# Kernel tuning notes

Measured on AMD Instinct MI355X. Metric: run time of the kernel, lower is better.

## Reference

```python
import jax, jax.numpy as jnp
import numpy as np

REL_LEN = 100  # self.relative_length in the module
LN_EPS = 1e-3  # tf.keras LayerNormalization default epsilon


def sinusoid_table(rel_len, d):
    # position_encoding_relative: sinusoid over relative offsets -L..L, [2L+1, d]
    pos = jnp.arange(-rel_len, rel_len + 1, dtype=jnp.float32)[:, None]
    i = jnp.arange(d // 2, dtype=jnp.float32)[None, :]
    inv_freq = jnp.exp(-jnp.log(10000.0) * (2.0 * i) / d)
    ang = pos * inv_freq
    return jnp.concatenate([jnp.sin(ang), jnp.cos(ang)], axis=-1)


def setup_inputs() -> dict:
    key = jax.random.key(0)
    B, S, E, HID, H = 4, 512, 512, 2048, 8
    ks = jax.random.split(key, 16)
    g = lambda k, sh: jax.random.normal(k, sh, jnp.float32) / jnp.sqrt(jnp.float32(sh[0]))
    return {
        "values": jax.random.normal(ks[0], (B, S, E), jnp.float32),
        "values_mask": jnp.ones((B, S), dtype=bool),
        "rel_enc": sinusoid_table(REL_LEN, E),            # [201, E]
        "ln0_g": jnp.ones((E,), jnp.float32), "ln0_b": jnp.zeros((E,), jnp.float32),
        "w_b0": g(ks[1], (E, HID)), "b_b0": jnp.zeros((HID,), jnp.float32),
        "wq": g(ks[2], (HID, E)), "bq": jnp.zeros((E,), jnp.float32),
        "wke": g(ks[3], (HID, E)), "bke": jnp.zeros((E,), jnp.float32),
        "wkv": g(ks[4], (HID, E)), "bkv": jnp.zeros((E,), jnp.float32),
        "wkr": g(ks[5], (E, E)), "bkr": jnp.zeros((E,), jnp.float32),
        "wab0": g(ks[6], (E, H)), "bab0": jnp.zeros((H,), jnp.float32),
        "wab1": g(ks[7], (E, H)), "bab1": jnp.zeros((H,), jnp.float32),
        "ln1_g": jnp.ones((E,), jnp.float32), "ln1_b": jnp.zeros((E,), jnp.float32),
        "w11": g(ks[8], (E, HID)), "b11": jnp.zeros((HID,), jnp.float32),
        "w12": g(ks[9], (HID, E)), "b12": jnp.zeros((E,), jnp.float32),
    }


def _ln(x, g, b):
    m = jnp.mean(x, -1, keepdims=True)
    v = jnp.var(x, -1, keepdims=True)
    return (x - m) * jax.lax.rsqrt(v + LN_EPS) * g + b


def reference(values, values_mask, rel_enc, ln0_g, ln0_b, w_b0, b_b0,
              wq, bq, wke, bke, wkv, bkv, wkr, bkr,
              wab0, bab0, wab1, bab1, ln1_g, ln1_b, w11, b11, w12, b12):
    B, S, E = values.shape
    H = wab0.shape[1]
    D = E // H
    # block0 (lastfc=False): LayerNorm -> Dense(hidden, relu)
    x = jax.nn.relu(_ln(values, ln0_g, ln0_b) @ w_b0 + b_b0)          # [B,S,HID]
    q = x @ wq + bq                                                    # [B,S,E]
    ke = x @ wke + bke
    kv = x @ wkv + bkv
    # relative encodings: gather = one-hot rel map @ encoding table
    offs = jnp.clip(jnp.arange(S)[None, :] - jnp.arange(S)[:, None], -REL_LEN, REL_LEN) + REL_LEN
    rel = rel_enc[offs]                                                # [S,S,E]
    kr = rel @ wkr + bkr                                               # [S,S,E]
    # learned bias terms
    bias0 = (ke @ wab0 + bab0).transpose(0, 2, 1)[:, :, None, :]       # [B,H,1,S]
    bias1 = (kr @ wab1 + bab1).transpose(2, 0, 1)[None]                # [1,H,S,S]
    tr = lambda u: u.reshape(B, S, H, D).transpose(0, 2, 1, 3)         # [B,H,S,D]
    qh, keh, kvh = tr(q), tr(ke), tr(kv)
    krh = kr.reshape(S, S, H, D).transpose(2, 0, 1, 3)                 # [H,S,S,D]
    # q . kr content-position term, contracted without [B,H,S,S,D] materialization
    biasprod = jnp.einsum('bhid,hijd->bhij', qh, krh)                  # [B,H,S,S]
    bias = biasprod + bias0 + bias1
    # AttentionWithBias: scaled dot product + bias, key mask + causal mask
    logits = jnp.einsum('bhid,bhjd->bhij', qh, keh) / jnp.sqrt(jnp.float32(D)) + bias
    causal = jnp.tril(jnp.ones((S, S), dtype=bool))[None, None]        # [1,1,S,S]
    keymask = values_mask[:, None, None, :]                            # [B,1,1,S]
    logits = jnp.where(causal & keymask, logits, jnp.float32(-1e9))
    scores = jax.nn.softmax(logits, axis=-1)
    att = jnp.einsum('bhij,bhjd->bhid', scores, kvh)                   # [B,H,S,D]
    att = att.transpose(0, 2, 1, 3).reshape(B, S, E)
    v = values + att
    # block1: LayerNorm -> Dense(hidden, relu) -> Dense(input_size)
    y = jax.nn.relu(_ln(v, ln1_g, ln1_b) @ w11 + b11) @ w12 + b12
    return v + y
```

## Files before the change

kernel.cpp:

```cpp
#include <hip/hip_runtime.h>
#include <hip/hip_bf16.h>
#include <cstddef>
#include <cstdint>

#define LN_EPS 0.001f

using short8 = __attribute__((ext_vector_type(8))) short;
using f32x4 = __attribute__((ext_vector_type(4))) float;

#define GLOAD_LDS16(gp, lp)                                                    \
  __builtin_amdgcn_global_load_lds(                                            \
      (const __attribute__((address_space(1))) void*)(gp),                     \
      (__attribute__((address_space(3))) void*)(lp), 16, 0, 0)

static __device__ __forceinline__ short f2bf(float x) {
  __hip_bfloat16 h = __float2bfloat16(x);
  return *reinterpret_cast<short*>(&h);
}

__global__ __launch_bounds__(256) void prep_ln_kernel(
    const float* __restrict__ w_b0, const float* __restrict__ w11,
    const float* __restrict__ wq, const float* __restrict__ wke,
    const float* __restrict__ wkv, const float* __restrict__ w12,
    const float* __restrict__ wkr, const float* __restrict__ rel_enc,
    __hip_bfloat16* __restrict__ w_b0t, __hip_bfloat16* __restrict__ w11t,
    __hip_bfloat16* __restrict__ wqt, __hip_bfloat16* __restrict__ wket,
    __hip_bfloat16* __restrict__ wkvt, __hip_bfloat16* __restrict__ w12t,
    __hip_bfloat16* __restrict__ wkrt, __hip_bfloat16* __restrict__ relb,
    const float* __restrict__ lnx, const float* __restrict__ lng,
    const float* __restrict__ lnb, __hip_bfloat16* __restrict__ lnout) {
  int bid = blockIdx.x;
  int t = threadIdx.x;
  if (bid >= 6656) {
    int row = bid - 6656;
    const float* xr = lnx + (size_t)row * 512;
    float v0 = xr[t], v1 = xr[t + 256];
    float s = v0 + v1, sq = v0 * v0 + v1 * v1;
#pragma unroll
    for (int o = 32; o; o >>= 1) {
      s += __shfl_down(s, o);
      sq += __shfl_down(sq, o);
    }
    __shared__ float wsum[4], wsq[4];
    __shared__ float mean_s, scale_s;
    int wid = t >> 6, lane = t & 63;
    if (lane == 0) { wsum[wid] = s; wsq[wid] = sq; }
    __syncthreads();
    if (t == 0) {
      float S = wsum[0] + wsum[1] + wsum[2] + wsum[3];
      float SQ = wsq[0] + wsq[1] + wsq[2] + wsq[3];
      float mean = S * (1.f / 512.f);
      float var = SQ * (1.f / 512.f) - mean * mean;
      mean_s = mean;
      scale_s = rsqrtf(var + LN_EPS);
    }
    __syncthreads();
    float mean = mean_s, scale = scale_s;
    __hip_bfloat16* orow = lnout + (size_t)row * 512;
    orow[t] = __float2bfloat16((v0 - mean) * scale * lng[t] + lnb[t]);
    orow[t + 256] = __float2bfloat16((v1 - mean) * scale * lng[t + 256] + lnb[t + 256]);
    return;
  }
  if (bid >= 6400) {
    int row = bid - 6400;
    float v0 = 0.f, v1 = 0.f;
    if (row < 201) {
      v0 = rel_enc[(size_t)row * 512 + t];
      v1 = rel_enc[(size_t)row * 512 + t + 256];
    }
    relb[(size_t)row * 512 + t] = __float2bfloat16(v0);
    relb[(size_t)row * 512 + t + 256] = __float2bfloat16(v1);
    return;
  }
  const float* in;
  __hip_bfloat16* outp;
  int R, C, bx, by;
  if (bid < 6144) {
    int seg = bid >> 10, idx = bid & 1023;
    if (seg == 0)      { in = w_b0; outp = w_b0t; R = 512;  C = 2048; }
    else if (seg == 1) { in = w11;  outp = w11t;  R = 512;  C = 2048; }
    else if (seg == 2) { in = wq;   outp = wqt;   R = 2048; C = 512;  }
    else if (seg == 3) { in = wke;  outp = wket;  R = 2048; C = 512;  }
    else if (seg == 4) { in = wkv;  outp = wkvt;  R = 2048; C = 512;  }
    else               { in = w12;  outp = w12t;  R = 2048; C = 512;  }
    if (R == 512) { bx = idx & 63; by = idx >> 6; }
    else          { bx = idx & 15; by = idx >> 4; }
  } else {
    int idx = bid - 6144;
    in = wkr; outp = wkrt; R = 512; C = 512;
    bx = idx & 15; by = idx >> 4;
  }
  __shared__ float tile[32][33];
  int c0 = bx * 32, r0 = by * 32;
  int tx = t & 31, ty = t >> 5;
#pragma unroll
  for (int p = 0; p < 4; p++) {
    int r = ty + p * 8;
    tile[r][tx] = in[(size_t)(r0 + r) * C + c0 + tx];
  }
  __syncthreads();
#pragma unroll
  for (int p = 0; p < 4; p++) {
    int r = ty + p * 8;
    outp[(size_t)(c0 + r) * R + r0 + tx] = __float2bfloat16(tile[tx][r]);
  }
}

__global__ __launch_bounds__(256) void ln_kernel(const float* __restrict__ x,
                                                 const float* __restrict__ g,
                                                 const float* __restrict__ bb,
                                                 __hip_bfloat16* __restrict__ out) {
  int row = blockIdx.x;
  const float* xr = x + (size_t)row * 512;
  int t = threadIdx.x;
  float v0 = xr[t], v1 = xr[t + 256];
  float s = v0 + v1, sq = v0 * v0 + v1 * v1;
#pragma unroll
  for (int o = 32; o; o >>= 1) {
    s += __shfl_down(s, o);
    sq += __shfl_down(sq, o);
  }
  __shared__ float wsum[4], wsq[4];
  __shared__ float mean_s, scale_s;
  int wid = t >> 6, lane = t & 63;
  if (lane == 0) { wsum[wid] = s; wsq[wid] = sq; }
  __syncthreads();
  if (t == 0) {
    float S = wsum[0] + wsum[1] + wsum[2] + wsum[3];
    float SQ = wsq[0] + wsq[1] + wsq[2] + wsq[3];
    float mean = S * (1.f / 512.f);
    float var = SQ * (1.f / 512.f) - mean * mean;
    mean_s = mean;
    scale_s = rsqrtf(var + LN_EPS);
  }
  __syncthreads();
  float mean = mean_s, scale = scale_s;
  __hip_bfloat16* orow = out + (size_t)row * 512;
  orow[t] = __float2bfloat16((v0 - mean) * scale * g[t] + bb[t]);
  orow[t + 256] = __float2bfloat16((v1 - mean) * scale * g[t + 256] + bb[t + 256]);
}

template <int TM, int TN, int MODE, int RELU, int RESID>
__global__ __launch_bounds__(256) void gemm_mfma(
    const __hip_bfloat16* __restrict__ A, const __hip_bfloat16* __restrict__ Bt,
    const float* __restrict__ bias0, const float* __restrict__ bias1,
    const float* __restrict__ bias2, const float* __restrict__ resid,
    void* __restrict__ out0, void* __restrict__ out1, void* __restrict__ out2,
    int M, int N, int K,
    const __hip_bfloat16* A2, const __hip_bfloat16* B2t,
    const float* bias_kr, void* out_kr, int ysplit) {
  constexpr int FM = TM / 32;
  constexpr int FN = TN / 32;
  __shared__ short As[2][TM * 64];
  __shared__ short Bs[2][TN * 64];
  int tid = threadIdx.x;
  int w = tid >> 6, lane = tid & 63;
  int wrow = (w >> 1) * (TM / 2);
  int wcol = (w & 1) * (TN / 2);
  int quad = lane >> 4, l16 = lane & 15;
  int bx = blockIdx.x, by = blockIdx.y;
  const short* Ag = (const short*)A;
  const short* Bg = (const short*)Bt;
  int N_ = N, K_ = K;
  bool is_kr = false;
  if (MODE == 1 && ysplit > 0 && by >= ysplit) {
    if (bx >= 512 / TN) return;
    is_kr = true;
    by -= ysplit;
    Ag = (const short*)A2;
    Bg = (const short*)B2t;
    N_ = 512;
    K_ = 512;
  }
  int row0 = by * TM, col0 = bx * TN;
  f32x4 acc[FM][FN];
#pragma unroll
  for (int i = 0; i < FM; i++)
#pragma unroll
    for (int j = 0; j < FN; j++) acc[i][j] = {0.f, 0.f, 0.f, 0.f};

  auto stage = [&](int k0, int buf) {
#pragma unroll
    for (int p = 0; p < TM / 32; p++) {
      int e = p * 256 + tid;
      int r = e >> 3, sc = e & 7;
      int c = sc ^ (r & 7);
      GLOAD_LDS16(Ag + (size_t)(row0 + r) * K_ + k0 + c * 8, &As[buf][e * 8]);
    }
#pragma unroll
    for (int p = 0; p < TN / 32; p++) {
      int e = p * 256 + tid;
      int r = e >> 3, sc = e & 7;
      int c = sc ^ (r & 7);
      GLOAD_LDS16(Bg + (size_t)(col0 + r) * K_ + k0 + c * 8, &Bs[buf][e * 8]);
    }
  };

  int nIter = K_ >> 6;
  stage(0, 0);
  for (int it = 0; it < nIter; ++it) {
    int cur = it & 1;
    __syncthreads();
    if (it + 1 < nIter) stage((it + 1) << 6, cur ^ 1);
#pragma unroll
    for (int u = 0; u < 2; u++) {
      short8 af[FM], bf[FN];
#pragma unroll
      for (int f = 0; f < FM; f++) {
        int r = wrow + f * 16 + l16;
        int slot = (u * 4 + quad) ^ (r & 7);
        af[f] = *(const short8*)&As[cur][(r * 8 + slot) * 8];
      }
#pragma unroll
      for (int f = 0; f < FN; f++) {
        int r = wcol + f * 16 + l16;
        int slot = (u * 4 + quad) ^ (r & 7);
        bf[f] = *(const short8*)&Bs[cur][(r * 8 + slot) * 8];
      }
#pragma unroll
      for (int fm = 0; fm < FM; fm++)
#pragma unroll
        for (int fn = 0; fn < FN; fn++)
          acc[fm][fn] = __builtin_amdgcn_mfma_f32_16x16x32_bf16(af[fm], bf[fn], acc[fm][fn], 0, 0, 0);
    }
  }

  int seg = 0;
  const float* bp = is_kr ? bias_kr : bias0;
  __hip_bfloat16* opb = nullptr;
  if (MODE == 2) {
    seg = col0 >> 9;
    bp = (seg == 0) ? bias0 : (seg == 1 ? bias1 : bias2);
    opb = (__hip_bfloat16*)((seg == 0) ? out0 : out1);
  }
#pragma unroll
  for (int fm = 0; fm < FM; fm++) {
#pragma unroll
    for (int fn = 0; fn < FN; fn++) {
      int gc = col0 + wcol + fn * 16 + l16;
      int bcol = (MODE == 2) ? (gc - seg * 512) : gc;
      float bv = bp[bcol];
#pragma unroll
      for (int r = 0; r < 4; r++) {
        int gr = row0 + wrow + fm * 16 + quad * 4 + r;
        float v = acc[fm][fn][r] + bv;
        if (RELU && !is_kr) v = fmaxf(v, 0.f);
        if (MODE == 0) {
          size_t idx = (size_t)gr * N_ + gc;
          if (RESID) v += resid[idx];
          ((float*)out0)[idx] = v;
        } else if (MODE == 1) {
          __hip_bfloat16* dst = is_kr ? (__hip_bfloat16*)out_kr : (__hip_bfloat16*)out0;
          dst[(size_t)gr * N_ + gc] = __float2bfloat16(v);
        } else {
          if (seg < 2) {
            opb[(size_t)gr * 512 + bcol] = __float2bfloat16(v);
          } else {
            int b_ = gr >> 9, s_ = gr & 511;
            int h_ = bcol >> 6, d_ = bcol & 63;
            ((__hip_bfloat16*)out2)[(size_t)((b_ * 8 + h_) * 64 + d_) * 512 + s_] =
                __float2bfloat16(v);
          }
        }
      }
    }
  }
}

__global__ void rowdot_merged(const __hip_bfloat16* __restrict__ ke,
                              const __hip_bfloat16* __restrict__ krtb,
                              const float* __restrict__ wab0, const float* __restrict__ bab0,
                              const float* __restrict__ wab1, const float* __restrict__ bab1,
                              float* __restrict__ keab, float* __restrict__ b1t) {
  int bid = blockIdx.x;
  int lane = threadIdx.x;
  int second = (bid >= 2048);
  int r = second ? (bid - 2048) : bid;
  const __hip_bfloat16* ar = (second ? krtb : ke) + (size_t)r * 512;
  const float* W = second ? wab1 : wab0;
  const float* bb = second ? bab1 : bab0;
  float a[8];
#pragma unroll
  for (int u = 0; u < 8; u++) a[u] = __bfloat162float(ar[lane + u * 64]);
  float s[8] = {0.f, 0.f, 0.f, 0.f, 0.f, 0.f, 0.f, 0.f};
#pragma unroll
  for (int u = 0; u < 8; u++) {
    int e = lane + u * 64;
    const float4* w4 = (const float4*)&W[(size_t)e * 8];
    float4 w0 = w4[0], w1 = w4[1];
    s[0] += a[u] * w0.x; s[1] += a[u] * w0.y; s[2] += a[u] * w0.z; s[3] += a[u] * w0.w;
    s[4] += a[u] * w1.x; s[5] += a[u] * w1.y; s[6] += a[u] * w1.z; s[7] += a[u] * w1.w;
  }
#pragma unroll
  for (int h = 0; h < 8; h++) {
    float v = s[h];
#pragma unroll
    for (int o = 1; o < 64; o <<= 1) v += __shfl_xor(v, o);
    if (lane == h) {
      if (!second) {
        int b_ = r >> 9, s_ = r & 511;
        keab[(size_t)(b_ * 8 + h) * 512 + s_] = v + bb[h];
      } else {
        b1t[(size_t)r * 8 + h] = v + bb[h];
      }
    }
  }
}

#define PST 136
__global__ __launch_bounds__(256) void attn_mfma4(
    const __hip_bfloat16* __restrict__ q, const __hip_bfloat16* __restrict__ ke,
    const __hip_bfloat16* __restrict__ kvt, const __hip_bfloat16* __restrict__ krtb,
    const float* __restrict__ keab, const float* __restrict__ b1t,
    const float* __restrict__ values, float* __restrict__ v_out) {
  const int S = 512, E = 512;
  __shared__ float bp[16 * 113];
  __shared__ short P[4][16 * PST];
  __shared__ float ml[4][32];
  int tid = threadIdx.x;
  int wave = tid >> 6, lane = tid & 63;
  int quad = lane >> 4, l16 = lane & 15;
  int band = 31 - blockIdx.x;
  int h = blockIdx.y, b = blockIdx.z;
  int wi0 = band * 16;

  const short* qg = (const short*)q;
  const short* keg = (const short*)ke;
  const short* kvtg = (const short*)kvt;
  const short* krg = (const short*)krtb;

  short8 aq[2];
#pragma unroll
  for (int kk = 0; kk < 2; kk++)
    aq[kk] = *(const short8*)&qg[(size_t)(b * S + wi0 + l16) * E + h * 64 + kk * 32 + quad * 8];

#pragma unroll
  for (int oi = 0; oi < 2; oi++) {
    int on = wave + oi * 4;
    if (on < 7) {
      f32x4 c = {0.f, 0.f, 0.f, 0.f};
#pragma unroll
      for (int kk = 0; kk < 2; kk++) {
        short8 bfr = *(const short8*)&krg[(size_t)(on * 16 + l16) * E + h * 64 + kk * 32 + quad * 8];
        c = __builtin_amdgcn_mfma_f32_16x16x32_bf16(aq[kk], bfr, c, 0, 0, 0);
      }
      float b1 = b1t[(on * 16 + l16) * 8 + h];
#pragma unroll
      for (int rr = 0; rr < 4; rr++)
        bp[(quad * 4 + rr) * 113 + on * 16 + l16] = c[rr] + b1;
    }
  }
  __syncthreads();

  int nb = (band >= wave) ? (((band - wave) >> 2) + 1) : 0;

  f32x4 s[8];
  const float* keabh = keab + (size_t)(b * 8 + h) * 512;
#pragma unroll
  for (int t = 0; t < 8; t++) {
    if (t < nb) {
      int j = (4 * t + wave) * 16 + l16;
      f32x4 c = {0.f, 0.f, 0.f, 0.f};
#pragma unroll
      for (int kk = 0; kk < 2; kk++) {
        short8 bk = *(const short8*)&keg[(size_t)(b * S + j) * E + h * 64 + kk * 32 + quad * 8];
        c = __builtin_amdgcn_mfma_f32_16x16x32_bf16(aq[kk], bk, c, 0, 0, 0);
      }
      float ka = keabh[j];
#pragma unroll
      for (int rr = 0; rr < 4; rr++) {
        int i = wi0 + quad * 4 + rr;
        float val = -1e30f;
        if (j <= i) {
          int off = j - i + 100;
          if (off < 0) off = 0;
          val = c[rr] * 0.125f + bp[(quad * 4 + rr) * 113 + off] + ka;
        }
        s[t][rr] = val;
      }
    }
  }

  float m_r[4] = {-1e30f, -1e30f, -1e30f, -1e30f};
#pragma unroll
  for (int t = 0; t < 8; t++)
    if (t < nb)
#pragma unroll
      for (int rr = 0; rr < 4; rr++) m_r[rr] = fmaxf(m_r[rr], s[t][rr]);
#pragma unroll
  for (int rr = 0; rr < 4; rr++) {
    float v = m_r[rr];
    v = fmaxf(v, __shfl_xor(v, 1));
    v = fmaxf(v, __shfl_xor(v, 2));
    v = fmaxf(v, __shfl_xor(v, 4));
    v = fmaxf(v, __shfl_xor(v, 8));
    m_r[rr] = v;
  }
  float l_r[4] = {0.f, 0.f, 0.f, 0.f};
  short* Pw = &P[wave][0];
#pragma unroll
  for (int t = 0; t < 8; t++) {
    if (t < nb) {
#pragma unroll
      for (int rr = 0; rr < 4; rr++) {
        float p = __expf(s[t][rr] - m_r[rr]);
        l_r[rr] += p;
        Pw[(quad * 4 + rr) * PST + t * 16 + l16] = f2bf(p);
      }
    }
  }
  if (nb & 1) {
#pragma unroll
    for (int rr = 0; rr < 4; rr++)
      Pw[(quad * 4 + rr) * PST + nb * 16 + l16] = 0;
  }
#pragma unroll
  for (int rr = 0; rr < 4; rr++) {
    float v = l_r[rr];
    v += __shfl_xor(v, 1);
    v += __shfl_xor(v, 2);
    v += __shfl_xor(v, 4);
    v += __shfl_xor(v, 8);
    l_r[rr] = v;
  }

  f32x4 o[4] = {{0.f,0.f,0.f,0.f},{0.f,0.f,0.f,0.f},{0.f,0.f,0.f,0.f},{0.f,0.f,0.f,0.f}};
  int nkk = (nb + 1) >> 1;
  const short* kvbase = &kvtg[(size_t)(b * 8 + h) * 64 * S];
#pragma unroll
  for (int kk = 0; kk < 4; kk++) {
    if (kk < nkk) {
      short8 ap = *(const short8*)&Pw[l16 * PST + kk * 32 + quad * 8];
      int jgl = (4 * (2 * kk + (quad >> 1)) + wave) * 16 + (quad & 1) * 8;
#pragma unroll
      for (int dn = 0; dn < 4; dn++) {
        short8 bv = *(const short8*)&kvbase[(size_t)(dn * 16 + l16) * S + jgl];
        o[dn] = __builtin_amdgcn_mfma_f32_16x16x32_bf16(ap, bv, o[dn], 0, 0, 0);
      }
    }
  }

  float* omw = (float*)&P[wave][0];
#pragma unroll
  for (int rr = 0; rr < 4; rr++) {
    int row = quad * 4 + rr;
    if (l16 == 0) {
      ml[wave][row * 2] = m_r[rr];
      ml[wave][row * 2 + 1] = l_r[rr];
    }
#pragma unroll
    for (int dn = 0; dn < 4; dn++)
      omw[row * 68 + dn * 16 + l16] = o[dn][rr];
  }
  __syncthreads();
  int dn = wave;
#pragma unroll
  for (int rr = 0; rr < 4; rr++) {
    int row = quad * 4 + rr;
    float ms = -1e30f;
#pragma unroll
    for (int wv = 0; wv < 4; wv++) ms = fmaxf(ms, ml[wv][row * 2]);
    float lsum = 0.f, oo = 0.f;
    int col = dn * 16 + l16;
#pragma unroll
    for (int wv = 0; wv < 4; wv++) {
      float aw = __expf(ml[wv][row * 2] - ms);
      lsum += ml[wv][row * 2 + 1] * aw;
      oo += ((float*)&P[wv][0])[row * 68 + col] * aw;
    }
    oo /= lsum;
    size_t idx = (size_t)(b * S + wi0 + row) * E + h * 64 + col;
    v_out[idx] = values[idx] + oo;
  }
}

extern "C" void kernel_launch(void* const* d_in, const int* in_sizes, int n_in,
                              void* d_out, int out_size, void* d_ws, size_t ws_size,
                              hipStream_t stream) {
  const float* values = (const float*)d_in[0];
  const float* rel_enc = (const float*)d_in[2];
  const float* ln0_g = (const float*)d_in[3];
  const float* ln0_b = (const float*)d_in[4];
  const float* w_b0 = (const float*)d_in[5];
  const float* b_b0 = (const float*)d_in[6];
  const float* wq = (const float*)d_in[7];
  const float* bq = (const float*)d_in[8];
  const float* wke = (const float*)d_in[9];
  const float* bke = (const float*)d_in[10];
  const float* wkv = (const float*)d_in[11];
  const float* bkv = (const float*)d_in[12];
  const float* wkr = (const float*)d_in[13];
  const float* bkr = (const float*)d_in[14];
  const float* wab0 = (const float*)d_in[15];
  const float* bab0 = (const float*)d_in[16];
  const float* wab1 = (const float*)d_in[17];
  const float* bab1 = (const float*)d_in[18];
  const float* ln1_g = (const float*)d_in[19];
  const float* ln1_b = (const float*)d_in[20];
  const float* w11 = (const float*)d_in[21];
  const float* b11 = (const float*)d_in[22];
  const float* w12 = (const float*)d_in[23];
  const float* b12 = (const float*)d_in[24];
  float* out = (float*)d_out;

  char* p = (char*)d_ws;
  __hip_bfloat16* buf_ln = (__hip_bfloat16*)p;  p += (size_t)2048 * 512 * 2;
  __hip_bfloat16* x      = (__hip_bfloat16*)p;  p += (size_t)2048 * 2048 * 2;
  __hip_bfloat16* q      = (__hip_bfloat16*)p;  p += (size_t)2048 * 512 * 2;
  __hip_bfloat16* ke     = (__hip_bfloat16*)p;  p += (size_t)2048 * 512 * 2;
  __hip_bfloat16* kvt    = (__hip_bfloat16*)p;  p += (size_t)2048 * 512 * 2;
  float* v    = (float*)p;                      p += (size_t)2048 * 512 * 4;
  __hip_bfloat16* krtb = (__hip_bfloat16*)p;    p += (size_t)256 * 512 * 2;
  __hip_bfloat16* relb = (__hip_bfloat16*)p;    p += (size_t)256 * 512 * 2;
  __hip_bfloat16* wkrt = (__hip_bfloat16*)p;    p += (size_t)512 * 512 * 2;
  float* keab = (float*)p;                      p += (size_t)4 * 8 * 512 * 4;
  float* b1t  = (float*)p;                      p += (size_t)208 * 8 * 4;
  __hip_bfloat16* w_b0t = (__hip_bfloat16*)p;   p += (size_t)2048 * 512 * 2;
  __hip_bfloat16* wcatt = (__hip_bfloat16*)p;   p += (size_t)1536 * 2048 * 2;
  __hip_bfloat16* w11t  = (__hip_bfloat16*)p;   p += (size_t)2048 * 512 * 2;
  __hip_bfloat16* w12t  = (__hip_bfloat16*)p;   p += (size_t)512 * 2048 * 2;

  __hip_bfloat16* wqt  = wcatt;
  __hip_bfloat16* wket = wcatt + (size_t)512 * 2048;
  __hip_bfloat16* wkvt = wcatt + (size_t)1024 * 2048;

  prep_ln_kernel<<<8704, 256, 0, stream>>>(w_b0, w11, wq, wke, wkv, w12, wkr, rel_enc,
                                           w_b0t, w11t, wqt, wket, wkvt, w12t, wkrt, relb,
                                           values, ln0_g, ln0_b, buf_ln);
  gemm_mfma<128, 64, 1, 1, 0><<<dim3(32, 18), 256, 0, stream>>>(
      buf_ln, w_b0t, b_b0, nullptr, nullptr, nullptr, x, nullptr, nullptr,
      2048, 2048, 512, relb, wkrt, bkr, krtb, 16);
  gemm_mfma<128, 64, 2, 0, 0><<<dim3(24, 16), 256, 0, stream>>>(
      x, wcatt, bq, bke, bkv, nullptr, q, ke, kvt, 2048, 1536, 2048,
      nullptr, nullptr, nullptr, nullptr, 0);
  rowdot_merged<<<2249, 64, 0, stream>>>(ke, krtb, wab0, bab0, wab1, bab1, keab, b1t);
  attn_mfma4<<<dim3(32, 8, 4), 256, 0, stream>>>(q, ke, kvt, krtb, keab, b1t, values, v);
  ln_kernel<<<2048, 256, 0, stream>>>(v, ln1_g, ln1_b, buf_ln);
  gemm_mfma<128, 64, 1, 1, 0><<<dim3(32, 16), 256, 0, stream>>>(
      buf_ln, w11t, b11, nullptr, nullptr, nullptr, x, nullptr, nullptr,
      2048, 2048, 512, nullptr, nullptr, nullptr, nullptr, 0);
  gemm_mfma<64, 64, 0, 0, 1><<<dim3(8, 32), 256, 0, stream>>>(
      x, w12t, b12, nullptr, nullptr, v, out, nullptr, nullptr, 2048, 512, 2048,
      nullptr, nullptr, nullptr, nullptr, 0);
}
```

Before: 227.3 us.

## Fuse per-head bias row-dots into GEMM epilogues via atomics, drop rowdot kernel

Removes the separate rowdot_merged kernel. The ke·wab0 and kr·wab1 per-head dot products are now computed in the epilogues of the projection GEMMs and accumulated into keab/b1t with atomicAdd, after the prep kernel pre-fills them with the biases. The kv transposed store is also packed into 64-bit writes. This saves one launch and a re-read of ke/kr, in exchange for extra epilogue work, float atomics, and dot products taken on fp32 values before bf16 rounding instead of on the stored bf16 values.

```diff
diff --git a/kernel.cpp b/kernel.cpp
--- a/kernel.cpp
+++ b/kernel.cpp
@@ -28,9 +28,21 @@
     __hip_bfloat16* __restrict__ wkvt, __hip_bfloat16* __restrict__ w12t,
     __hip_bfloat16* __restrict__ wkrt, __hip_bfloat16* __restrict__ relb,
     const float* __restrict__ lnx, const float* __restrict__ lng,
-    const float* __restrict__ lnb, __hip_bfloat16* __restrict__ lnout) {
+    const float* __restrict__ lnb, __hip_bfloat16* __restrict__ lnout,
+    const float* __restrict__ bab0, const float* __restrict__ bab1,
+    float* __restrict__ keab, float* __restrict__ b1t) {
   int bid = blockIdx.x;
   int t = threadIdx.x;
+  if (bid >= 8768) {
+    int idx = (bid - 8768) * 256 + t;
+    if (idx < 208 * 8) b1t[idx] = bab1[idx & 7];
+    return;
+  }
+  if (bid >= 8704) {
+    int idx = (bid - 8704) * 256 + t;
+    keab[idx] = bab0[(idx >> 9) & 7];
+    return;
+  }
   if (bid >= 6656) {
     int row = bid - 6656;
     const float* xr = lnx + (size_t)row * 512;
@@ -140,7 +152,7 @@
   orow[t + 256] = __float2bfloat16((v1 - mean) * scale * g[t + 256] + bb[t + 256]);
 }
 
-template <int TM, int TN, int MODE, int RELU, int RESID>
+template <int TM, int TN, int MODE, int RELU, int RESID, int DOT>
 __global__ __launch_bounds__(256) void gemm_mfma(
     const __hip_bfloat16* __restrict__ A, const __hip_bfloat16* __restrict__ Bt,
     const float* __restrict__ bias0, const float* __restrict__ bias1,
@@ -148,7 +160,8 @@
     void* __restrict__ out0, void* __restrict__ out1, void* __restrict__ out2,
     int M, int N, int K,
     const __hip_bfloat16* A2, const __hip_bfloat16* B2t,
-    const float* bias_kr, void* out_kr, int ysplit) {
+    const float* bias_kr, void* out_kr, int ysplit,
+    const float* wdot0, float* dot0, const float* wdot1, float* dot1) {
   constexpr int FM = TM / 32;
   constexpr int FN = TN / 32;
   __shared__ short As[2][TM * 64];
@@ -225,83 +238,115 @@
     }
   }
 
-  int seg = 0;
-  const float* bp = is_kr ? bias_kr : bias0;
-  __hip_bfloat16* opb = nullptr;
   if (MODE == 2) {
-    seg = col0 >> 9;
-    bp = (seg == 0) ? bias0 : (seg == 1 ? bias1 : bias2);
-    opb = (__hip_bfloat16*)((seg == 0) ? out0 : out1);
-  }
-#pragma unroll
-  for (int fm = 0; fm < FM; fm++) {
-#pragma unroll
-    for (int fn = 0; fn < FN; fn++) {
-      int gc = col0 + wcol + fn * 16 + l16;
-      int bcol = (MODE == 2) ? (gc - seg * 512) : gc;
-      float bv = bp[bcol];
+    int seg = col0 >> 9;
+    const float* bp = (seg == 0) ? bias0 : (seg == 1 ? bias1 : bias2);
+    if (seg < 2) {
+      __hip_bfloat16* dst = (__hip_bfloat16*)(seg == 0 ? out0 : out1);
+#pragma unroll
+      for (int fm = 0; fm < FM; fm++) {
+#pragma unroll
+        for (int r = 0; r < 4; r++) {
+          int gr = row0 + wrow + fm * 16 + quad * 4 + r;
+          float dotp[8] = {0.f, 0.f, 0.f, 0.f, 0.f, 0.f, 0.f, 0.f};
+#pragma unroll
+          for (int fn = 0; fn < FN; fn++) {
+            int gc = col0 + wcol + fn * 16 + l16;
+            int bcol = gc - seg * 512;
+            float v = acc[fm][fn][r] + bp[bcol];
+            dst[(size_t)gr * 512 + bcol] = __float2bfloat16(v);
+            if (DOT && seg == 1) {
+              const float4* wv = (const float4*)&wdot0[(size_t)bcol * 8];
+              float4 w0 = wv[0], w1 = wv[1];
+              dotp[0] += v * w0.x; dotp[1] += v * w0.y; dotp[2] += v * w0.z; dotp[3] += v * w0.w;
+              dotp[4] += v * w1.x; dotp[5] += v * w1.y; dotp[6] += v * w1.z; dotp[7] += v * w1.w;
+            }
+          }
+          if (DOT && seg == 1) {
+#pragma unroll
+            for (int h = 0; h < 8; h++) {
+              float d = dotp[h];
+              d += __shfl_xor(d, 1);
+              d += __shfl_xor(d, 2);
+              d += __shfl_xor(d, 4);
+              d += __shfl_xor(d, 8);
+              if (l16 == 0) {
+                int b_ = gr >> 9, s_ = gr & 511;
+                atomicAdd(&dot0[(size_t)(b_ * 8 + h) * 512 + s_], d);
+              }
+            }
+          }
+        }
+      }
+    } else {
+#pragma unroll
+      for (int fm = 0; fm < FM; fm++) {
+#pragma unroll
+        for (int fn = 0; fn < FN; fn++) {
+          int gc = col0 + wcol + fn * 16 + l16;
+          int bcol = gc - 1024;
+          float bv = bp[bcol];
+          int gr0 = row0 + wrow + fm * 16 + quad * 4;
+          union { unsigned long long u; short s4[4]; } pk;
+#pragma unroll
+          for (int r = 0; r < 4; r++) pk.s4[r] = f2bf(acc[fm][fn][r] + bv);
+          int b_ = gr0 >> 9, s_ = gr0 & 511;
+          int h_ = bcol >> 6, d_ = bcol & 63;
+          *(unsigned long long*)&((short*)out2)[(size_t)((b_ * 8 + h_) * 64 + d_) * 512 + s_] = pk.u;
+        }
+      }
+    }
+  } else if (MODE == 1) {
+    const float* bp = is_kr ? bias_kr : bias0;
+    __hip_bfloat16* dst = is_kr ? (__hip_bfloat16*)out_kr : (__hip_bfloat16*)out0;
+#pragma unroll
+    for (int fm = 0; fm < FM; fm++) {
 #pragma unroll
       for (int r = 0; r < 4; r++) {
         int gr = row0 + wrow + fm * 16 + quad * 4 + r;
-        float v = acc[fm][fn][r] + bv;
-        if (RELU && !is_kr) v = fmaxf(v, 0.f);
-        if (MODE == 0) {
+        float dotp[8] = {0.f, 0.f, 0.f, 0.f, 0.f, 0.f, 0.f, 0.f};
+#pragma unroll
+        for (int fn = 0; fn < FN; fn++) {
+          int gc = col0 + wcol + fn * 16 + l16;
+          float v = acc[fm][fn][r] + bp[gc];
+          if (RELU && !is_kr) v = fmaxf(v, 0.f);
+          dst[(size_t)gr * N_ + gc] = __float2bfloat16(v);
+          if (DOT && is_kr) {
+            const float4* wv = (const float4*)&wdot1[(size_t)gc * 8];
+            float4 w0 = wv[0], w1 = wv[1];
+            dotp[0] += v * w0.x; dotp[1] += v * w0.y; dotp[2] += v * w0.z; dotp[3] += v * w0.w;
+            dotp[4] += v * w1.x; dotp[5] += v * w1.y; dotp[6] += v * w1.z; dotp[7] += v * w1.w;
+          }
+        }
+        if (DOT && is_kr) {
+#pragma unroll
+          for (int h = 0; h < 8; h++) {
+            float d = dotp[h];
+            d += __shfl_xor(d, 1);
+            d += __shfl_xor(d, 2);
+            d += __shfl_xor(d, 4);
+            d += __shfl_xor(d, 8);
+            if (l16 == 0 && gr < 208) atomicAdd(&dot1[gr * 8 + h], d);
+          }
+        }
+      }
+    }
+  } else {
+#pragma unroll
+    for (int fm = 0; fm < FM; fm++) {
+#pragma unroll
+      for (int fn = 0; fn < FN; fn++) {
+        int gc = col0 + wcol + fn * 16 + l16;
+        float bv = bias0[gc];
+#pragma unroll
+        for (int r = 0; r < 4; r++) {
+          int gr = row0 + wrow + fm * 16 + quad * 4 + r;
+          float v = acc[fm][fn][r] + bv;
+          if (RELU) v = fmaxf(v, 0.f);
           size_t idx = (size_t)gr * N_ + gc;
           if (RESID) v += resid[idx];
           ((float*)out0)[idx] = v;
-        } else if (MODE == 1) {
-          __hip_bfloat16* dst = is_kr ? (__hip_bfloat16*)out_kr : (__hip_bfloat16*)out0;
-          dst[(size_t)gr * N_ + gc] = __float2bfloat16(v);
-        } else {
-          if (seg < 2) {
-            opb[(size_t)gr * 512 + bcol] = __float2bfloat16(v);
-          } else {
-            int b_ = gr >> 9, s_ = gr & 511;
-            int h_ = bcol >> 6, d_ = bcol & 63;
-            ((__hip_bfloat16*)out2)[(size_t)((b_ * 8 + h_) * 64 + d_) * 512 + s_] =
-                __float2bfloat16(v);
-          }
         }
-      }
-    }
-  }
-}
-
-__global__ void rowdot_merged(const __hip_bfloat16* __restrict__ ke,
-                              const __hip_bfloat16* __restrict__ krtb,
-                              const float* __restrict__ wab0, const float* __restrict__ bab0,
-                              const float* __restrict__ wab1, const float* __restrict__ bab1,
-                              float* __restrict__ keab, float* __restrict__ b1t) {
-  int bid = blockIdx.x;
-  int lane = threadIdx.x;
-  int second = (bid >= 2048);
-  int r = second ? (bid - 2048) : bid;
-  const __hip_bfloat16* ar = (second ? krtb : ke) + (size_t)r * 512;
-  const float* W = second ? wab1 : wab0;
-  const float* bb = second ? bab1 : bab0;
-  float a[8];
-#pragma unroll
-  for (int u = 0; u < 8; u++) a[u] = __bfloat162float(ar[lane + u * 64]);
-  float s[8] = {0.f, 0.f, 0.f, 0.f, 0.f, 0.f, 0.f, 0.f};
-#pragma unroll
-  for (int u = 0; u < 8; u++) {
-    int e = lane + u * 64;
-    const float4* w4 = (const float4*)&W[(size_t)e * 8];
-    float4 w0 = w4[0], w1 = w4[1];
-    s[0] += a[u] * w0.x; s[1] += a[u] * w0.y; s[2] += a[u] * w0.z; s[3] += a[u] * w0.w;
-    s[4] += a[u] * w1.x; s[5] += a[u] * w1.y; s[6] += a[u] * w1.z; s[7] += a[u] * w1.w;
-  }
-#pragma unroll
-  for (int h = 0; h < 8; h++) {
-    float v = s[h];
-#pragma unroll
-    for (int o = 1; o < 64; o <<= 1) v += __shfl_xor(v, o);
-    if (lane == h) {
-      if (!second) {
-        int b_ = r >> 9, s_ = r & 511;
-        keab[(size_t)(b_ * 8 + h) * 512 + s_] = v + bb[h];
-      } else {
-        b1t[(size_t)r * 8 + h] = v + bb[h];
       }
     }
   }
@@ -524,22 +569,26 @@
   __hip_bfloat16* wket = wcatt + (size_t)512 * 2048;
   __hip_bfloat16* wkvt = wcatt + (size_t)1024 * 2048;
 
-  prep_ln_kernel<<<8704, 256, 0, stream>>>(w_b0, w11, wq, wke, wkv, w12, wkr, rel_enc,
+  prep_ln_kernel<<<8775, 256, 0, stream>>>(w_b0, w11, wq, wke, wkv, w12, wkr, rel_enc,
                                            w_b0t, w11t, wqt, wket, wkvt, w12t, wkrt, relb,
-                                           values, ln0_g, ln0_b, buf_ln);
-  gemm_mfma<128, 64, 1, 1, 0><<<dim3(32, 18), 256, 0, stream>>>(
+                                           values, ln0_g, ln0_b, buf_ln,
+                                           bab0, bab1, keab, b1t);
+  gemm_mfma<128, 64, 1, 1, 0, 1><<<dim3(32, 18), 256, 0, stream>>>(
       buf_ln, w_b0t, b_b0, nullptr, nullptr, nullptr, x, nullptr, nullptr,
-      2048, 2048, 512, relb, wkrt, bkr, krtb, 16);
-  gemm_mfma<128, 64, 2, 0, 0><<<dim3(24, 16), 256, 0, stream>>>(
+      2048, 2048, 512, relb, wkrt, bkr, krtb, 16,
+      nullptr, nullptr, wab1, b1t);
+  gemm_mfma<128, 64, 2, 0, 0, 1><<<dim3(24, 16), 256, 0, stream>>>(
       x, wcatt, bq, bke, bkv, nullptr, q, ke, kvt, 2048, 1536, 2048,
-      nullptr, nullptr, nullptr, nullptr, 0);
-  rowdot_merged<<<2249, 64, 0, stream>>>(ke, krtb, wab0, bab0, wab1, bab1, keab, b1t);
+      nullptr, nullptr, nullptr, nullptr, 0,
+      wab0, keab, nullptr, nullptr);
   attn_mfma4<<<dim3(32, 8, 4), 256, 0, stream>>>(q, ke, kvt, krtb, keab, b1t, values, v);
   ln_kernel<<<2048, 256, 0, stream>>>(v, ln1_g, ln1_b, buf_ln);
-  gemm_mfma<128, 64, 1, 1, 0><<<dim3(32, 16), 256, 0, stream>>>(
+  gemm_mfma<128, 64, 1, 1, 0, 0><<<dim3(32, 16), 256, 0, stream>>>(
       buf_ln, w11t, b11, nullptr, nullptr, nullptr, x, nullptr, nullptr,
-      2048, 2048, 512, nullptr, nullptr, nullptr, nullptr, 0);
-  gemm_mfma<64, 64, 0, 0, 1><<<dim3(8, 32), 256, 0, stream>>>(
+      2048, 2048, 512, nullptr, nullptr, nullptr, nullptr, 0,
+      nullptr, nullptr, nullptr, nullptr);
+  gemm_mfma<64, 64, 0, 0, 1, 0><<<dim3(8, 32), 256, 0, stream>>>(
       x, w12t, b12, nullptr, nullptr, v, out, nullptr, nullptr, 2048, 512, 2048,
-      nullptr, nullptr, nullptr, nullptr, 0);
+      nullptr, nullptr, nullptr, nullptr, 0,
+      nullptr, nullptr, nullptr, nullptr);
 }
```

Result: slower. 282.8 us (+24.4%).
